# Performance work log

Hardware: AMD Instinct MI355X
Metric: run time of the kernel (lower is better)

## Reference

```python
import jax, jax.numpy as jnp
import numpy as np

N_NODES = 50000
N_EDGES = 1600000
N_FEAT = 4
N_GRAPHS = 128
K = 5


def setup_inputs() -> dict:
    key = jax.random.key(0)
    ks = jax.random.split(key, 16)
    x = jax.random.normal(ks[0], (N_NODES, N_FEAT), dtype=jnp.float32)
    edge_index = jax.random.randint(ks[1], (2, N_EDGES), 0, N_NODES, dtype=jnp.int64)
    batch = jnp.sort(jax.random.randint(ks[2], (N_NODES,), 0, N_GRAPHS, dtype=jnp.int64))
    def lin(k, shape):
        fan_in = shape[-2]
        return jax.random.normal(k, shape, dtype=jnp.float32) / np.sqrt(fan_in)
    return {
        "x": x,
        "edge_index": edge_index,
        "batch": batch,
        "num_graphs": N_GRAPHS,
        "W1": lin(ks[3], (K, N_FEAT, 32)), "b1": jnp.zeros((32,), jnp.float32),
        "W2": lin(ks[4], (K, 32, 64)),     "b2": jnp.zeros((64,), jnp.float32),
        "W3": lin(ks[5], (K, 64, 64)),     "b3": jnp.zeros((64,), jnp.float32),
        "fcw1": lin(ks[6], (64, 32)), "fcb1": jnp.zeros((32,), jnp.float32),
        "fcw2": lin(ks[7], (32, 1)),  "fcb2": jnp.zeros((1,), jnp.float32),
    }


def _cheb_conv(h, src, dst, w, Wk, b, n_nodes):
    # PyG ChebConv with sym norm, lambda_max=2:
    #   L_hat h = scatter_add(w_e * h[src_e] -> dst_e), w_e = -dinv[src]*dinv[dst]
    def L(z):
        return jax.ops.segment_sum(w[:, None] * z[src], dst, num_segments=n_nodes)
    Tx0 = h
    Tx1 = L(h)
    out = jnp.einsum('nf,fo->no', Tx0, Wk[0]) + jnp.einsum('nf,fo->no', Tx1, Wk[1])
    for k in range(2, Wk.shape[0]):
        Tx2 = 2.0 * L(Tx1) - Tx0
        out = out + jnp.einsum('nf,fo->no', Tx2, Wk[k])
        Tx0, Tx1 = Tx1, Tx2
    return out + b


def reference(x, edge_index, batch, num_graphs, W1, b1, W2, b2, W3, b3,
              fcw1, fcb1, fcw2, fcb2):
    n = x.shape[0]
    src, dst = edge_index[0], edge_index[1]
    # remove self loops (PyG ChebConv does remove_self_loops first)
    ew = (src != dst).astype(x.dtype)
    deg = jax.ops.segment_sum(ew, src, num_segments=n)
    dinv = jnp.where(deg > 0, jax.lax.rsqrt(jnp.where(deg > 0, deg, 1.0)), 0.0)
    w = -ew * dinv[src] * dinv[dst]  # scaled Laplacian off-diagonal; diagonal is 0

    h = jax.nn.relu(_cheb_conv(x, src, dst, w, W1, b1, n))
    h = jax.nn.relu(_cheb_conv(h, src, dst, w, W2, b2, n))
    h = jax.nn.relu(_cheb_conv(h, src, dst, w, W3, b3, n))

    # global_mean_pool over graph segments
    sums = jax.ops.segment_sum(h, batch, num_segments=num_graphs)
    cnts = jax.ops.segment_sum(jnp.ones((n,), h.dtype), batch, num_segments=num_graphs)
    pooled = sums / jnp.maximum(cnts, 1.0)[:, None]

    h = jax.nn.relu(pooled @ fcw1 + fcb1)
    return h @ fcw2 + fcb2
```

## Files before the change

kernel.cpp:

```cpp
#include <hip/hip_runtime.h>


constexpr int N_NODES  = 50000;
constexpr int N_EDGES  = 1600000;
constexpr int N_GRAPHS = 128;

constexpr int NB_H = 256;
constexpr int EPB  = N_EDGES / NB_H;
constexpr int NW   = (N_NODES + 3) / 4;

static inline int cdiv(long long a, int b) { return (int)((a + b - 1) / b); }


template <int USE_DST>
__global__ __launch_bounds__(256) void hist_kernel(const int* __restrict__ src,
                                                   const int* __restrict__ dst,
                                                   unsigned* __restrict__ H) {
    __shared__ unsigned lds[NW];
    const int b = blockIdx.x, t = threadIdx.x;
    for (int i = t; i < NW; i += 256) lds[i] = 0;
    __syncthreads();
    const int e0 = b * EPB, e1 = e0 + EPB;
    for (int e = e0 + t; e < e1; e += 256) {
        int s = src[e], d = dst[e];
        if (s != d) {
            int key = USE_DST ? d : s;
            atomicAdd(&lds[key >> 2], 1u << (8 * (key & 3)));
        }
    }
    __syncthreads();
    unsigned* Hb = H + (size_t)b * NW;
    for (int i = t; i < NW; i += 256) Hb[i] = lds[i];
}

__global__ void merge_src_kernel(const unsigned* __restrict__ H, float* __restrict__ dinv) {
    int i = blockIdx.x * blockDim.x + threadIdx.x;
    if (i >= NW) return;
    unsigned s0 = 0, s1 = 0, s2 = 0, s3 = 0;
    for (int b = 0; b < NB_H; ++b) {
        unsigned v = H[(size_t)b * NW + i];
        s0 += v & 0xff; s1 += (v >> 8) & 0xff; s2 += (v >> 16) & 0xff; s3 += v >> 24;
    }
    dinv[4 * i + 0] = s0 ? rsqrtf((float)s0) : 0.f;
    dinv[4 * i + 1] = s1 ? rsqrtf((float)s1) : 0.f;
    dinv[4 * i + 2] = s2 ? rsqrtf((float)s2) : 0.f;
    dinv[4 * i + 3] = s3 ? rsqrtf((float)s3) : 0.f;
}

__global__ void merge_dst_kernel(const unsigned* __restrict__ H, unsigned* __restrict__ P,
                                 int* __restrict__ cnt) {
    int i = blockIdx.x * blockDim.x + threadIdx.x;
    if (i >= NW) return;
    unsigned p0 = 0, p1 = 0, p2 = 0, p3 = 0;
    for (int b = 0; b < NB_H; ++b) {
        size_t idx = (size_t)b * NW + i;
        unsigned v = H[idx];
        P[idx] = p0 | (p1 << 8) | (p2 << 16) | (p3 << 24);
        p0 += v & 0xff; p1 += (v >> 8) & 0xff; p2 += (v >> 16) & 0xff; p3 += v >> 24;
    }
    cnt[4 * i + 0] = (int)p0; cnt[4 * i + 1] = (int)p1;
    cnt[4 * i + 2] = (int)p2; cnt[4 * i + 3] = (int)p3;
}


constexpr int SCAN_B = 256;
constexpr int SCAN_NB = (N_NODES + SCAN_B - 1) / SCAN_B;

__global__ void scan_block_kernel(const int* __restrict__ cnt, int* __restrict__ row,
                                  int* __restrict__ bsum) {
    __shared__ int buf[SCAN_B];
    int t = threadIdx.x;
    int i = blockIdx.x * SCAN_B + t;
    buf[t] = (i < N_NODES) ? cnt[i] : 0;
    __syncthreads();
    for (int off = 1; off < SCAN_B; off <<= 1) {
        int a = (t >= off) ? buf[t - off] : 0;
        __syncthreads();
        buf[t] += a;
        __syncthreads();
    }
    if (i < N_NODES) row[i + 1] = buf[t];
    if (t == SCAN_B - 1) bsum[blockIdx.x] = buf[t];
    if (i == 0) row[0] = 0;
}

__global__ void scan_sums_kernel(int* __restrict__ bsum) {
    __shared__ int buf[SCAN_NB];
    int t = threadIdx.x;
    if (t < SCAN_NB) buf[t] = bsum[t];
    __syncthreads();
    for (int off = 1; off < SCAN_NB; off <<= 1) {
        int a = (t >= off && t < SCAN_NB) ? buf[t - off] : 0;
        __syncthreads();
        if (t < SCAN_NB) buf[t] += a;
        __syncthreads();
    }
    if (t < SCAN_NB) bsum[t] = buf[t];
}

__global__ void scan_add_kernel(int* __restrict__ row, const int* __restrict__ bsum) {
    int i = blockIdx.x * SCAN_B + threadIdx.x;
    if (blockIdx.x > 0 && i < N_NODES) row[i + 1] += bsum[blockIdx.x - 1];
}

__global__ __launch_bounds__(256) void place_kernel(const int* __restrict__ src,
                                                    const int* __restrict__ dst,
                                                    const float* __restrict__ dinv,
                                                    const int* __restrict__ row,
                                                    const unsigned* __restrict__ P,
                                                    float2* __restrict__ csr) {
    __shared__ unsigned lds[NW];
    const int b = blockIdx.x, t = threadIdx.x;
    for (int i = t; i < NW; i += 256) lds[i] = 0;
    __syncthreads();
    const int e0 = b * EPB, e1 = e0 + EPB;
    const unsigned* Pb = P + (size_t)b * NW;
    for (int e = e0 + t; e < e1; e += 256) {
        int s = src[e], d = dst[e];
        if (s != d) {
            float w = -dinv[s] * dinv[d];
            int sh = 8 * (d & 3);
            unsigned old = atomicAdd(&lds[d >> 2], 1u << sh);
            unsigned cur = (old >> sh) & 0xff;
            unsigned pref = (Pb[d >> 2] >> sh) & 0xff;
            int pos = row[d] + (int)pref + (int)cur;
            csr[pos] = make_float2(w, __int_as_float(s));
        }
    }
}


template <int F>
__global__ void gather_kernel(const int* __restrict__ row, const float2* __restrict__ csr,
                              const float* __restrict__ z, const float* __restrict__ prev,
                              float* __restrict__ out, float alpha, float beta) {
    constexpr int NPB = 256 / F;
    int node = blockIdx.x * NPB + threadIdx.x / F;
    int lane = threadIdx.x % F;
    if (node >= N_NODES) return;
    int e0 = row[node], e1 = row[node + 1];
    float acc = 0.f;
#pragma unroll 4
    for (int e = e0; e < e1; ++e) {
        float2 ew = csr[e];
        acc = fmaf(ew.x, z[(size_t)__float_as_int(ew.y) * F + lane], acc);
    }
    float r = alpha * acc;
    if (beta != 0.f) r = fmaf(beta, prev[(size_t)node * F + lane], r);
    out[(size_t)node * F + lane] = r;
}

__global__ void gather4_kernel(const int* __restrict__ row, const float2* __restrict__ csr,
                               const float* __restrict__ z, const float* __restrict__ prev,
                               float* __restrict__ out, float alpha, float beta) {
    int node = blockIdx.x * blockDim.x + threadIdx.x;
    if (node >= N_NODES) return;
    int e0 = row[node], e1 = row[node + 1];
    const float4* z4 = (const float4*)z;
    float4 a = make_float4(0.f, 0.f, 0.f, 0.f);
#pragma unroll 4
    for (int e = e0; e < e1; ++e) {
        float2 ew = csr[e];
        float4 zz = z4[__float_as_int(ew.y)];
        a.x = fmaf(ew.x, zz.x, a.x);
        a.y = fmaf(ew.x, zz.y, a.y);
        a.z = fmaf(ew.x, zz.z, a.z);
        a.w = fmaf(ew.x, zz.w, a.w);
    }
    float4 r = make_float4(alpha * a.x, alpha * a.y, alpha * a.z, alpha * a.w);
    if (beta != 0.f) {
        const float4 p = ((const float4*)prev)[node];
        r.x = fmaf(beta, p.x, r.x);
        r.y = fmaf(beta, p.y, r.y);
        r.z = fmaf(beta, p.z, r.z);
        r.w = fmaf(beta, p.w, r.w);
    }
    ((float4*)out)[node] = r;
}


template <int FI>
__global__ __launch_bounds__(256, 4) void combine64_kernel(
        const float* __restrict__ X, const float* __restrict__ T1,
        const float* __restrict__ T2, const float* __restrict__ T3,
        const float* __restrict__ T4, const float* __restrict__ W,
        const float* __restrict__ b, float* __restrict__ out) {
    constexpr int FO = 64;
    constexpr int TS = FI + 4;
    __shared__ float Ts[64 * TS];
    __shared__ float Ws[FI * FO];
    const int t = threadIdx.x;
    const int tn = t & 15;
    const int to = t >> 4;
    const int n_base = blockIdx.x * 64;
    const float* Tk[5] = {X, T1, T2, T3, T4};

    float acc[4][4];
    {
        const float4 bb = *(const float4*)(b + 4 * to);
#pragma unroll
        for (int i = 0; i < 4; ++i) {
            acc[i][0] = bb.x; acc[i][1] = bb.y; acc[i][2] = bb.z; acc[i][3] = bb.w;
        }
    }

#pragma unroll
    for (int k = 0; k < 5; ++k) {
        __syncthreads();
        {
            const float4* s4 = (const float4*)(Tk[k] + (size_t)n_base * FI);
            constexpr int NV = 64 * FI / 4;
#pragma unroll
            for (int idx = t; idx < NV; idx += 256) {
                int r = idx / (FI / 4), c = idx % (FI / 4);
                float4 v = make_float4(0.f, 0.f, 0.f, 0.f);
                if (n_base + r < N_NODES) v = s4[idx];
                *(float4*)(Ts + r * TS + 4 * c) = v;
            }
            const float4* w4 = (const float4*)(W + (size_t)k * FI * FO);
            constexpr int WV = FI * FO / 4;
#pragma unroll
            for (int idx = t; idx < WV; idx += 256) *(float4*)(Ws + 4 * idx) = w4[idx];
        }
        __syncthreads();
#pragma unroll 4
        for (int f0 = 0; f0 < FI; f0 += 4) {
            float tv[4][4];
#pragma unroll
            for (int i = 0; i < 4; ++i) {
                float4 q = *(const float4*)(Ts + (tn + 16 * i) * TS + f0);
                tv[i][0] = q.x; tv[i][1] = q.y; tv[i][2] = q.z; tv[i][3] = q.w;
            }
#pragma unroll
            for (int j = 0; j < 4; ++j) {
                float4 w = *(const float4*)(Ws + (f0 + j) * FO + 4 * to);
#pragma unroll
                for (int i = 0; i < 4; ++i) {
                    acc[i][0] = fmaf(tv[i][j], w.x, acc[i][0]);
                    acc[i][1] = fmaf(tv[i][j], w.y, acc[i][1]);
                    acc[i][2] = fmaf(tv[i][j], w.z, acc[i][2]);
                    acc[i][3] = fmaf(tv[i][j], w.w, acc[i][3]);
                }
            }
        }
    }
    __syncthreads();
#pragma unroll
    for (int i = 0; i < 4; ++i) {
        int n = n_base + tn + 16 * i;
        if (n < N_NODES) {
            float4 r = make_float4(fmaxf(acc[i][0], 0.f), fmaxf(acc[i][1], 0.f),
                                   fmaxf(acc[i][2], 0.f), fmaxf(acc[i][3], 0.f));
            *(float4*)(out + (size_t)n * FO + 4 * to) = r;
        }
    }
}

__global__ void combine432_kernel(const float* __restrict__ X, const float* __restrict__ T1,
                                  const float* __restrict__ T2, const float* __restrict__ T3,
                                  const float* __restrict__ T4, const float* __restrict__ W,
                                  const float* __restrict__ b, float* __restrict__ out) {
    __shared__ float Ws[5 * 4 * 32];
    int t = threadIdx.x;
    for (int i = t; i < 5 * 4 * 32; i += 256) Ws[i] = W[i];
    __syncthreads();
    int node = blockIdx.x * 8 + (t >> 5);
    int o = t & 31;
    if (node >= N_NODES) return;
    const float4* Tk[5] = {(const float4*)X, (const float4*)T1, (const float4*)T2,
                           (const float4*)T3, (const float4*)T4};
    float acc = b[o];
#pragma unroll
    for (int k = 0; k < 5; ++k) {
        float4 q = Tk[k][node];
        const float* w = Ws + k * 128 + o;
        acc = fmaf(q.x, w[0], acc);
        acc = fmaf(q.y, w[32], acc);
        acc = fmaf(q.z, w[64], acc);
        acc = fmaf(q.w, w[96], acc);
    }
    out[(size_t)node * 32 + o] = fmaxf(acc, 0.f);
}


__global__ void pool_kernel(const float* __restrict__ h, const int* __restrict__ batch,
                            float* __restrict__ pooled, float* __restrict__ cntf) {
    int wid = blockIdx.x * (blockDim.x / 64) + (threadIdx.x >> 6);
    int lane = threadIdx.x & 63;
    int nwaves = gridDim.x * (blockDim.x / 64);
    int per = (N_NODES + nwaves - 1) / nwaves;
    int n0 = wid * per;
    int n1 = min(n0 + per, N_NODES);
    if (n0 >= n1) return;
    int cur = batch[n0];
    float acc = 0.f;
    int c = 0;
    for (int n = n0; n < n1; ++n) {
        int g = batch[n];
        if (g != cur) {
            atomicAdd(&pooled[cur * 64 + lane], acc);
            if (lane == 0) atomicAdd(&cntf[cur], (float)c);
            acc = 0.f; c = 0; cur = g;
        }
        acc += h[(size_t)n * 64 + lane];
        ++c;
    }
    atomicAdd(&pooled[cur * 64 + lane], acc);
    if (lane == 0) atomicAdd(&cntf[cur], (float)c);
}

__global__ void fc_kernel(const float* __restrict__ pooled, const float* __restrict__ cnt,
                          const float* __restrict__ w1, const float* __restrict__ b1,
                          const float* __restrict__ w2, const float* __restrict__ b2,
                          float* __restrict__ out) {
    int g = blockIdx.x;
    int t = threadIdx.x;
    __shared__ float hid[32];
    float c = fmaxf(cnt[g], 1.0f);
    float acc = b1[t];
    for (int f = 0; f < 64; ++f) acc = fmaf(pooled[g * 64 + f] / c, w1[f * 32 + t], acc);
    hid[t] = fmaxf(acc, 0.f);
    __syncthreads();
    if (t == 0) {
        float acc2 = b2[0];
        for (int o = 0; o < 32; ++o) acc2 = fmaf(hid[o], w2[o], acc2);
        out[g] = acc2;
    }
}


template <int FI, int FO>
static void run_layer(const int* row, const float2* csr, const float* X,
                      float* T1, float* T2, float* T3, float* T4,
                      const float* W, const float* b, float* out, hipStream_t stream) {
    if constexpr (FI == 4) {
        dim3 g(cdiv(N_NODES, 256)), blk(256);
        hipLaunchKernelGGL(gather4_kernel, g, blk, 0, stream, row, csr, X,  X,  T1, 1.f, 0.f);
        hipLaunchKernelGGL(gather4_kernel, g, blk, 0, stream, row, csr, T1, X,  T2, 2.f, -1.f);
        hipLaunchKernelGGL(gather4_kernel, g, blk, 0, stream, row, csr, T2, T1, T3, 2.f, -1.f);
        hipLaunchKernelGGL(gather4_kernel, g, blk, 0, stream, row, csr, T3, T2, T4, 2.f, -1.f);
    } else {
        constexpr int NPB = 256 / FI;
        dim3 g(cdiv(N_NODES, NPB)), blk(256);
        hipLaunchKernelGGL((gather_kernel<FI>), g, blk, 0, stream, row, csr, X,  X,  T1, 1.f, 0.f);
        hipLaunchKernelGGL((gather_kernel<FI>), g, blk, 0, stream, row, csr, T1, X,  T2, 2.f, -1.f);
        hipLaunchKernelGGL((gather_kernel<FI>), g, blk, 0, stream, row, csr, T2, T1, T3, 2.f, -1.f);
        hipLaunchKernelGGL((gather_kernel<FI>), g, blk, 0, stream, row, csr, T3, T2, T4, 2.f, -1.f);
    }
    if constexpr (FO == 64) {
        hipLaunchKernelGGL((combine64_kernel<FI>), dim3(cdiv(N_NODES, 64)), dim3(256), 0,
                           stream, X, T1, T2, T3, T4, W, b, out);
    } else {
        hipLaunchKernelGGL(combine432_kernel, dim3(cdiv(N_NODES, 8)), dim3(256), 0,
                           stream, X, T1, T2, T3, T4, W, b, out);
    }
}

extern "C" void kernel_launch(void* const* d_in, const int* in_sizes, int n_in,
                              void* d_out, int out_size, void* d_ws, size_t ws_size,
                              hipStream_t stream) {
    const float* x    = (const float*)d_in[0];
    const int*   ei   = (const int*)d_in[1];
    const int*   batch= (const int*)d_in[2];
    const float* W1   = (const float*)d_in[4];
    const float* b1   = (const float*)d_in[5];
    const float* W2   = (const float*)d_in[6];
    const float* b2   = (const float*)d_in[7];
    const float* W3   = (const float*)d_in[8];
    const float* b3   = (const float*)d_in[9];
    const float* fcw1 = (const float*)d_in[10];
    const float* fcb1 = (const float*)d_in[11];
    const float* fcw2 = (const float*)d_in[12];
    const float* fcb2 = (const float*)d_in[13];

    const int* src = ei;
    const int* dst = ei + N_EDGES;

    float* base = (float*)d_ws;
    float*  dinv   = base + 0;
    int*    cnt_i  = (int*)(base + 50000);
    int*    row    = (int*)(base + 100000);
    int*    bsum   = (int*)(base + 150004);
    float2* csr    = (float2*)(base + 150256);
    float*  T1     = base + 3350256;
    float*  T2     = base + 6550256;
    float*  T3     = base + 9750256;
    float*  T4     = base + 12950256;
    float*  H1     = T4 + 1600000;
    float*  H2     = base + 16150256;
    float*  pooled = base + 19350256;
    float*  cntf   = base + 19358448;

    unsigned* Hs = (unsigned*)T1;
    unsigned* Hd = (unsigned*)T2;
    unsigned* P  = (unsigned*)T3;

    hipLaunchKernelGGL((hist_kernel<0>), dim3(NB_H), dim3(256), 0, stream, src, dst, Hs);
    hipLaunchKernelGGL((hist_kernel<1>), dim3(NB_H), dim3(256), 0, stream, src, dst, Hd);
    hipLaunchKernelGGL(merge_src_kernel, dim3(cdiv(NW, 256)), dim3(256), 0, stream, Hs, dinv);
    hipLaunchKernelGGL(merge_dst_kernel, dim3(cdiv(NW, 256)), dim3(256), 0, stream, Hd, P, cnt_i);
    hipLaunchKernelGGL(scan_block_kernel, dim3(SCAN_NB), dim3(SCAN_B), 0, stream, cnt_i, row, bsum);
    hipLaunchKernelGGL(scan_sums_kernel, dim3(1), dim3(256), 0, stream, bsum);
    hipLaunchKernelGGL(scan_add_kernel, dim3(SCAN_NB), dim3(SCAN_B), 0, stream, row, bsum);
    hipLaunchKernelGGL(place_kernel, dim3(NB_H), dim3(256), 0, stream,
                       src, dst, dinv, row, P, csr);

    run_layer<4, 32>(row, csr, x,  T1, T2, T3, T4, W1, b1, H1, stream);
    run_layer<32, 64>(row, csr, H1, T1, T2, T3, T4, W2, b2, H2, stream);
    run_layer<64, 64>(row, csr, H2, T1, T2, T3, T4, W3, b3, T1, stream);

    hipMemsetAsync(pooled, 0, (8192 + 128) * sizeof(float), stream);
    hipLaunchKernelGGL(pool_kernel, dim3(128), dim3(256), 0, stream, T1, batch, pooled, cntf);
    hipLaunchKernelGGL(fc_kernel, dim3(N_GRAPHS), dim3(32), 0, stream,
                       pooled, cntf, fcw1, fcb1, fcw2, fcb2, (float*)d_out);
}
```

Baseline: 805.9 us.

## Store features as 16-wide slices and map slices to XCDs in gather

```diff
diff --git a/kernel.cpp b/kernel.cpp
--- a/kernel.cpp
+++ b/kernel.cpp
@@ -4,6 +4,9 @@
 constexpr int N_NODES  = 50000;
 constexpr int N_EDGES  = 1600000;
 constexpr int N_GRAPHS = 128;
+
+constexpr int N16  = N_NODES * 16;
+constexpr int SB16 = (N_NODES + 15) / 16;
 
 constexpr int NB_H = 256;
 constexpr int EPB  = N_EDGES / NB_H;
@@ -129,26 +132,6 @@
     }
 }
 
-
-template <int F>
-__global__ void gather_kernel(const int* __restrict__ row, const float2* __restrict__ csr,
-                              const float* __restrict__ z, const float* __restrict__ prev,
-                              float* __restrict__ out, float alpha, float beta) {
-    constexpr int NPB = 256 / F;
-    int node = blockIdx.x * NPB + threadIdx.x / F;
-    int lane = threadIdx.x % F;
-    if (node >= N_NODES) return;
-    int e0 = row[node], e1 = row[node + 1];
-    float acc = 0.f;
-#pragma unroll 4
-    for (int e = e0; e < e1; ++e) {
-        float2 ew = csr[e];
-        acc = fmaf(ew.x, z[(size_t)__float_as_int(ew.y) * F + lane], acc);
-    }
-    float r = alpha * acc;
-    if (beta != 0.f) r = fmaf(beta, prev[(size_t)node * F + lane], r);
-    out[(size_t)node * F + lane] = r;
-}
 
 __global__ void gather4_kernel(const int* __restrict__ row, const float2* __restrict__ csr,
                                const float* __restrict__ z, const float* __restrict__ prev,
@@ -178,6 +161,37 @@
     ((float4*)out)[node] = r;
 }
 
+template <int NSLICE>
+__global__ __launch_bounds__(256) void gather16_kernel(
+        const int* __restrict__ row, const float2* __restrict__ csr,
+        const float* __restrict__ z, const float* __restrict__ prev,
+        float* __restrict__ out, float alpha, float beta) {
+    constexpr int XPS = 8 / NSLICE;
+    const int bid = blockIdx.x;
+    const int xcd = bid & 7;
+    const int slice = xcd / XPS;
+    const int sblk = (bid >> 3) * XPS + (xcd % XPS);
+    if (sblk >= SB16) return;
+    const int t = threadIdx.x;
+    const int n = sblk * 16 + (t >> 4);
+    const int lane = t & 15;
+    const float* zs = z + (size_t)slice * N16;
+    const int e0 = row[n], e1 = row[n + 1];
+    float acc = 0.f;
+#pragma unroll 4
+    for (int e = e0; e < e1; ++e) {
+        unsigned long long raw =
+            __builtin_nontemporal_load((const unsigned long long*)csr + e);
+        float w = __uint_as_float((unsigned)raw);
+        int s = (int)(raw >> 32);
+        acc = fmaf(w, zs[(size_t)s * 16 + lane], acc);
+    }
+    float r = alpha * acc;
+    size_t off = (size_t)slice * N16 + (size_t)n * 16 + lane;
+    if (beta != 0.f) r = fmaf(beta, __builtin_nontemporal_load(prev + off), r);
+    out[off] = r;
+}
+
 
 template <int FI>
 __global__ __launch_bounds__(256, 4) void combine64_kernel(
@@ -208,13 +222,17 @@
     for (int k = 0; k < 5; ++k) {
         __syncthreads();
         {
-            const float4* s4 = (const float4*)(Tk[k] + (size_t)n_base * FI);
+            const float* base = Tk[k];
             constexpr int NV = 64 * FI / 4;
 #pragma unroll
             for (int idx = t; idx < NV; idx += 256) {
                 int r = idx / (FI / 4), c = idx % (FI / 4);
+                int s = c >> 2;
+                int j = (c & 3) * 4;
                 float4 v = make_float4(0.f, 0.f, 0.f, 0.f);
-                if (n_base + r < N_NODES) v = s4[idx];
+                if (n_base + r < N_NODES)
+                    v = *(const float4*)(base + (size_t)s * N16 +
+                                         (size_t)(n_base + r) * 16 + j);
                 *(float4*)(Ts + r * TS + 4 * c) = v;
             }
             const float4* w4 = (const float4*)(W + (size_t)k * FI * FO);
@@ -251,7 +269,9 @@
         if (n < N_NODES) {
             float4 r = make_float4(fmaxf(acc[i][0], 0.f), fmaxf(acc[i][1], 0.f),
                                    fmaxf(acc[i][2], 0.f), fmaxf(acc[i][3], 0.f));
-            *(float4*)(out + (size_t)n * FO + 4 * to) = r;
+            int s = to >> 2;
+            int j = (to & 3) * 4;
+            *(float4*)(out + (size_t)s * N16 + (size_t)n * 16 + j) = r;
         }
     }
 }
@@ -279,7 +299,7 @@
         acc = fmaf(q.z, w[64], acc);
         acc = fmaf(q.w, w[96], acc);
     }
-    out[(size_t)node * 32 + o] = fmaxf(acc, 0.f);
+    out[(size_t)(o >> 4) * N16 + (size_t)node * 16 + (o & 15)] = fmaxf(acc, 0.f);
 }
 
 
@@ -292,6 +312,7 @@
     int n0 = wid * per;
     int n1 = min(n0 + per, N_NODES);
     if (n0 >= n1) return;
+    const float* hp = h + (size_t)(lane >> 4) * N16 + (lane & 15);
     int cur = batch[n0];
     float acc = 0.f;
     int c = 0;
@@ -302,7 +323,7 @@
             if (lane == 0) atomicAdd(&cntf[cur], (float)c);
             acc = 0.f; c = 0; cur = g;
         }
-        acc += h[(size_t)n * 64 + lane];
+        acc += hp[(size_t)n * 16];
         ++c;
     }
     atomicAdd(&pooled[cur * 64 + lane], acc);
@@ -340,12 +361,13 @@
         hipLaunchKernelGGL(gather4_kernel, g, blk, 0, stream, row, csr, T2, T1, T3, 2.f, -1.f);
         hipLaunchKernelGGL(gather4_kernel, g, blk, 0, stream, row, csr, T3, T2, T4, 2.f, -1.f);
     } else {
-        constexpr int NPB = 256 / FI;
-        dim3 g(cdiv(N_NODES, NPB)), blk(256);
-        hipLaunchKernelGGL((gather_kernel<FI>), g, blk, 0, stream, row, csr, X,  X,  T1, 1.f, 0.f);
-        hipLaunchKernelGGL((gather_kernel<FI>), g, blk, 0, stream, row, csr, T1, X,  T2, 2.f, -1.f);
-        hipLaunchKernelGGL((gather_kernel<FI>), g, blk, 0, stream, row, csr, T2, T1, T3, 2.f, -1.f);
-        hipLaunchKernelGGL((gather_kernel<FI>), g, blk, 0, stream, row, csr, T3, T2, T4, 2.f, -1.f);
+        constexpr int NSLICE = FI / 16;
+        constexpr int XPS = 8 / NSLICE;
+        dim3 g(cdiv(SB16, XPS) * 8), blk(256);
+        hipLaunchKernelGGL((gather16_kernel<NSLICE>), g, blk, 0, stream, row, csr, X,  X,  T1, 1.f, 0.f);
+        hipLaunchKernelGGL((gather16_kernel<NSLICE>), g, blk, 0, stream, row, csr, T1, X,  T2, 2.f, -1.f);
+        hipLaunchKernelGGL((gather16_kernel<NSLICE>), g, blk, 0, stream, row, csr, T2, T1, T3, 2.f, -1.f);
+        hipLaunchKernelGGL((gather16_kernel<NSLICE>), g, blk, 0, stream, row, csr, T3, T2, T4, 2.f, -1.f);
     }
     if constexpr (FO == 64) {
         hipLaunchKernelGGL((combine64_kernel<FI>), dim3(cdiv(N_NODES, 64)), dim3(256), 0,
```

New measurement: 1.023 ms. +27.0%, slower.
